# Kernel optimization log

Hardware: AMD Instinct MI355X
Metric: run time of the kernel (lower is better)

The kernel has to match this reference:

```python
import jax, jax.numpy as jnp
import numpy as np

N_NODES = 100000
E_HALF = 2000000  # edges come in two mirrored halves (two classes per node pair)
IN_DIM, HID = 5, 16


def setup_inputs() -> dict:
    key = jax.random.key(0)
    ks = jax.random.split(key, 8)
    x = jax.random.normal(ks[0], (N_NODES, IN_DIM), dtype=jnp.float32)
    e_half = jax.random.randint(ks[1], (2, E_HALF), 0, N_NODES)
    edges = jnp.concatenate([e_half, e_half], axis=1)  # [2, 2*E_HALF]
    edge_attr = jax.random.uniform(ks[2], (2 * E_HALF, 2), dtype=jnp.float32)
    detector_labels = jax.random.bernoulli(ks[3], 0.5, (N_NODES,))
    s = 1.0 / np.sqrt(IN_DIM)
    W_rel = jax.random.uniform(ks[4], (HID, IN_DIM), minval=-s, maxval=s, dtype=jnp.float32)
    b_rel = jax.random.uniform(ks[5], (HID,), minval=-s, maxval=s, dtype=jnp.float32)
    W_root = jax.random.uniform(ks[6], (HID, IN_DIM), minval=-s, maxval=s, dtype=jnp.float32)
    s2 = 1.0 / np.sqrt(2 * HID + 1)
    k7, k8 = jax.random.split(ks[7])
    W_lin = jax.random.uniform(k7, (1, 2 * HID + 1), minval=-s2, maxval=s2, dtype=jnp.float32)
    b_lin = jax.random.uniform(k8, (1,), minval=-s2, maxval=s2, dtype=jnp.float32)
    return {
        "x": x, "edges": edges, "edge_attr": edge_attr,
        "detector_labels": detector_labels,
        "W_rel": W_rel, "b_rel": b_rel, "W_root": W_root,
        "W_lin": W_lin, "b_lin": b_lin,
    }


def reference(x, edges, edge_attr, detector_labels, W_rel, b_rel, W_root, W_lin, b_lin):
    N = x.shape[0]
    src, dst = edges[0], edges[1]
    # GraphConv(aggr='add'): out_i = W_root x_i + W_rel * sum_{(j->i)} w_e * x_j + b_rel
    w = edge_attr[:, 1]
    msg = x[src] * w[:, None]                                  # [E, 5]
    agg = jax.ops.segment_sum(msg, dst, num_segments=N)        # [N, 5]
    h = jnp.tanh(agg @ W_rel.T + b_rel + x @ W_root.T)         # [N, 16]
    # SplitSyndromes: keep edges whose both endpoints are detector nodes
    valid = detector_labels[src] & detector_labels[dst]
    vidx = jnp.nonzero(valid)[0]                               # data-dependent (eager)
    e = edges[:, vidx]
    ea = edge_attr[vidx]
    # gather-concat-linear edge scoring
    feat = jnp.concatenate([h[e[0]], ea[:, :1], h[e[1]]], axis=-1)  # [nv, 33]
    score = feat @ W_lin.T + b_lin                             # [nv, 1]
    nv = score.shape[0]
    half = nv // 2
    score2 = score.reshape(-1, half)                           # [2, half]
    classes2 = ea[:, 1].reshape(-1, half)
    mi = jnp.argmin(score2, axis=0)
    cols = jnp.arange(half)
    return e[:, :half], score2[mi, cols], classes2[mi, cols]
```

## Files before the change

kernel.cpp:

```cpp
#include <hip/hip_runtime.h>

#define HID 16
#define IN_DIM 5
#define PAD 8
#define EPT 4
#define EPB (256 * EPT)

#define FXS 64.0f
#define FXI 0.015625f

__device__ __forceinline__ float decode_field(unsigned long long& T) {
    int r = (int)(T & 0xFFFull);
    int s = (r >= 2048) ? r - 4096 : r;
    T = (T - (unsigned long long)(long long)s) >> 12;
    return (float)s * FXI;
}

__device__ __forceinline__ void scan256(const int* __restrict__ counts,
                                        int* __restrict__ offs, int nbv) {
    __shared__ int wS[4];
    int tid = threadIdx.x;
    int base = tid * 8;
    int vals[8];
    int tsum = 0;
#pragma unroll
    for (int k = 0; k < 8; k++) {
        int idx = base + k;
        vals[k] = (idx < nbv) ? counts[idx] : 0;
        tsum += vals[k];
    }
    int lane = tid & 63, wid = tid >> 6;
    int scan = tsum;
#pragma unroll
    for (int off = 1; off < 64; off <<= 1) {
        int u = __shfl_up(scan, off, 64);
        if (lane >= off) scan += u;
    }
    if (lane == 63) wS[wid] = scan;
    __syncthreads();
    int waveBase = 0;
#pragma unroll
    for (int k = 0; k < 4; k++) if (k < wid) waveBase += wS[k];
    int excl = waveBase + scan - tsum;
#pragma unroll
    for (int k = 0; k < 8; k++) {
        int idx = base + k;
        if (idx < nbv) offs[idx] = excl;
        excl += vals[k];
    }
}

__device__ __forceinline__ void gridbar(int* bar, int G) {
    __syncthreads();
    if (threadIdx.x == 0) {
        __threadfence();
        __hip_atomic_fetch_add(bar, 1, __ATOMIC_ACQ_REL, __HIP_MEMORY_SCOPE_AGENT);
        while (__hip_atomic_load(bar, __ATOMIC_ACQUIRE, __HIP_MEMORY_SCOPE_AGENT) < G)
            __builtin_amdgcn_s_sleep(32);
        __threadfence();
    }
    __syncthreads();
}

__global__ __launch_bounds__(256) void fused(
        const float* __restrict__ x, const int* __restrict__ src,
        const int* __restrict__ dst, const float2* __restrict__ ea2,
        const int* __restrict__ lab,
        const float* __restrict__ Wrel, const float* __restrict__ brel,
        const float* __restrict__ Wroot, const float* __restrict__ Wlin,
        const float* __restrict__ blin,
        unsigned long long* __restrict__ agg, float2* __restrict__ uvp,
        int* __restrict__ counts, int* __restrict__ offs,
        float4* __restrict__ st4, float* __restrict__ out,
        int* __restrict__ bars,
        int N, int EH, int K, int nbv) {
    const int tid = threadIdx.x;
    const int G = gridDim.x;
    const int GT = G * 256;
    const int gt = blockIdx.x * 256 + tid;
    const int lane = tid & 63, wid = tid >> 6;

    __shared__ float sWrel[HID * IN_DIM];
    __shared__ float sWroot[HID * IN_DIM];
    __shared__ float sBrel[HID];
    __shared__ float sWl[2 * HID + 1];
    if (tid < HID * IN_DIM) sWrel[tid] = Wrel[tid];
    else if (tid < 2 * HID * IN_DIM) sWroot[tid - HID * IN_DIM] = Wroot[tid - HID * IN_DIM];
    else if (tid < 2 * HID * IN_DIM + HID) sBrel[tid - 2 * HID * IN_DIM] = brel[tid - 2 * HID * IN_DIM];
    else if (tid < 2 * HID * IN_DIM + HID + 2 * HID + 1)
        sWl[tid - 2 * HID * IN_DIM - HID] = Wlin[tid - 2 * HID * IN_DIM - HID];

    float w16 = Wlin[HID];
    __shared__ int wc[4];
    for (int vb = blockIdx.x; vb < nbv; vb += G) {
        const int i0 = vb * EPB + tid * EPT;
        int s[EPT], d[EPT];
        float2 eaA[EPT], eaB[EPT];
        bool act[EPT];
        if (i0 + EPT <= EH) {
            int4 s4 = *(const int4*)(src + i0);
            int4 d4 = *(const int4*)(dst + i0);
            s[0] = s4.x; s[1] = s4.y; s[2] = s4.z; s[3] = s4.w;
            d[0] = d4.x; d[1] = d4.y; d[2] = d4.z; d[3] = d4.w;
            float4 a0 = *(const float4*)(ea2 + i0);
            float4 a1 = *(const float4*)(ea2 + i0 + 2);
            float4 b0 = *(const float4*)(ea2 + (size_t)i0 + EH);
            float4 b1 = *(const float4*)(ea2 + (size_t)i0 + EH + 2);
            eaA[0] = make_float2(a0.x, a0.y); eaA[1] = make_float2(a0.z, a0.w);
            eaA[2] = make_float2(a1.x, a1.y); eaA[3] = make_float2(a1.z, a1.w);
            eaB[0] = make_float2(b0.x, b0.y); eaB[1] = make_float2(b0.z, b0.w);
            eaB[2] = make_float2(b1.x, b1.y); eaB[3] = make_float2(b1.z, b1.w);
#pragma unroll
            for (int k = 0; k < EPT; k++) act[k] = true;
        } else {
#pragma unroll
            for (int k = 0; k < EPT; k++) {
                int i = i0 + k;
                act[k] = (i < EH);
                s[k] = act[k] ? src[i] : 0;
                d[k] = act[k] ? dst[i] : 0;
                eaA[k] = act[k] ? ea2[i] : make_float2(0.f, 0.f);
                eaB[k] = act[k] ? ea2[(size_t)i + EH] : make_float2(0.f, 0.f);
            }
        }
        bool ld[EPT], vl[EPT];
#pragma unroll
        for (int k = 0; k < EPT; k++) {
            bool ls = lab[s[k]] != 0;
            bool lv = lab[d[k]] != 0;
            ld[k] = act[k] && lv;
            vl[k] = ld[k] && ls;
        }
#pragma unroll
        for (int k = 0; k < EPT; k++) {
            if (ld[k]) {
                const float* xs = x + (size_t)s[k] * IN_DIM;
                float4 xa = *(const float4*)xs;
                float  x4 = xs[4];
                float w = (eaA[k].y + eaB[k].y) * FXS;
                unsigned long long a = 0;
                int q0 = __float2int_rn(xa.x * w);
                int q1 = __float2int_rn(xa.y * w);
                int q2 = __float2int_rn(xa.z * w);
                int q3 = __float2int_rn(xa.w * w);
                int q4 = __float2int_rn(x4 * w);
                a += (unsigned long long)(long long)q0;
                a += (unsigned long long)(long long)q1 << 12;
                a += (unsigned long long)(long long)q2 << 24;
                a += (unsigned long long)(long long)q3 << 36;
                a += (unsigned long long)(long long)q4 << 48;
                atomicAdd(&agg[(size_t)d[k] * PAD], a);
            }
        }
        float scpart[EPT], cls[EPT];
#pragma unroll
        for (int k = 0; k < EPT; k++) {
            float p0 = w16 * eaA[k].x;
            float p1 = w16 * eaB[k].x;
            if (p1 < p0) { scpart[k] = p1; cls[k] = eaB[k].y; }
            else         { scpart[k] = p0; cls[k] = eaA[k].y; }
        }
        unsigned m4 = 0;
#pragma unroll
        for (int k = 0; k < EPT; k++) m4 |= (vl[k] ? (1u << k) : 0u);
        int cnt = __popc(m4);
        int scan = cnt;
#pragma unroll
        for (int off = 1; off < 64; off <<= 1) {
            int u = __shfl_up(scan, off, 64);
            if (lane >= off) scan += u;
        }
        __syncthreads();
        if (lane == 63) wc[wid] = scan;
        __syncthreads();
        if (tid == 0) counts[vb] = wc[0] + wc[1] + wc[2] + wc[3];
        int wexcl = 0;
#pragma unroll
        for (int k = 0; k < 4; k++) if (k < wid) wexcl += wc[k];
        int idx = vb * EPB + wexcl + (scan - cnt);
#pragma unroll
        for (int k = 0; k < EPT; k++) {
            if (vl[k]) {
                float4 r;
                r.x = __int_as_float(s[k]);
                r.y = __int_as_float(d[k]);
                r.z = scpart[k];
                r.w = cls[k];
                st4[idx++] = r;
            }
        }
    }
    gridbar(&bars[0], G);

    if (blockIdx.x == 0) scan256(counts, offs, nbv);
    {
        int iters = (N + GT - 1) / GT;
        for (int it = 0; it < iters; ++it) {
            int n = gt + it * GT;
            if (n < N && lab[n]) {
                unsigned long long T = agg[(size_t)n * PAD];
                float a[IN_DIM], xv[IN_DIM];
#pragma unroll
                for (int dd = 0; dd < IN_DIM; dd++) a[dd] = decode_field(T);
#pragma unroll
                for (int dd = 0; dd < IN_DIM; dd++) xv[dd] = x[(size_t)n * IN_DIM + dd];
                float u = 0.f, vv = 0.f;
#pragma unroll
                for (int kk = 0; kk < HID; kk++) {
                    float acc = sBrel[kk];
#pragma unroll
                    for (int dd = 0; dd < IN_DIM; dd++)
                        acc += a[dd] * sWrel[kk * IN_DIM + dd] + xv[dd] * sWroot[kk * IN_DIM + dd];
                    float hk = tanhf(acc);
                    u += sWl[kk] * hk;
                    vv += sWl[HID + 1 + kk] * hk;
                }
                uvp[n] = make_float2(u, vv);
            }
        }
    }
    gridbar(&bars[16], G);

    float bl = blin[0];
    const float* uvf = (const float*)uvp;
    for (int vb = blockIdx.x; vb < nbv; vb += G) {
        int cnt = counts[vb];
        int base = offs[vb];
        for (int t = tid; t < cnt; t += 256) {
            float4 r = st4[(size_t)vb * EPB + t];
            int s = __float_as_int(r.x);
            int d = __float_as_int(r.y);
            float sc = bl + uvf[2 * (size_t)s] + uvf[2 * (size_t)d + 1] + r.z;
            int ro = base + t;
            out[ro] = (float)s;
            out[(size_t)K + ro] = (float)d;
            out[2 * (size_t)K + ro] = sc;
            out[3 * (size_t)K + ro] = r.w;
        }
    }
}

__global__ void pack_labels(const int* __restrict__ lab, const float* __restrict__ x,
                            unsigned long long* __restrict__ bits, float* __restrict__ xp,
                            int N) {
    int n = blockIdx.x * 256 + threadIdx.x;
    bool p = (n < N) && (lab[n] != 0);
    unsigned long long m = __ballot(p);
    if (((threadIdx.x & 63) == 0) && n < N) bits[n >> 6] = m;
    if (n < N) {
        float4 a;
        a.x = x[(size_t)n * IN_DIM + 0];
        a.y = x[(size_t)n * IN_DIM + 1];
        a.z = x[(size_t)n * IN_DIM + 2];
        a.w = x[(size_t)n * IN_DIM + 3];
        *(float4*)(xp + (size_t)n * 8) = a;
        float4 b;
        b.x = x[(size_t)n * IN_DIM + 4];
        b.y = 0.f; b.z = 0.f; b.w = 0.f;
        *(float4*)(xp + (size_t)n * 8 + 4) = b;
    }
}

__global__ __launch_bounds__(256, 4) void scatter_count(
        const int* __restrict__ src, const int* __restrict__ dst,
        const unsigned long long* __restrict__ bits,
        const float2* __restrict__ ea2,
        const float* __restrict__ xp,
        const float* __restrict__ Wlin,
        unsigned long long* __restrict__ agg,
        int* __restrict__ counts,
        float4* __restrict__ st4,
        int EH) {
    const int tid = threadIdx.x;
    const int i0 = (blockIdx.x * 256 + tid) * EPT;
    int s[EPT], d[EPT];
    float2 eaA[EPT], eaB[EPT];
    bool act[EPT];
    if (i0 + EPT <= EH) {
        int4 s4 = *(const int4*)(src + i0);
        int4 d4 = *(const int4*)(dst + i0);
        s[0] = s4.x; s[1] = s4.y; s[2] = s4.z; s[3] = s4.w;
        d[0] = d4.x; d[1] = d4.y; d[2] = d4.z; d[3] = d4.w;
        float4 a0 = *(const float4*)(ea2 + i0);
        float4 a1 = *(const float4*)(ea2 + i0 + 2);
        float4 b0 = *(const float4*)(ea2 + (size_t)i0 + EH);
        float4 b1 = *(const float4*)(ea2 + (size_t)i0 + EH + 2);
        eaA[0] = make_float2(a0.x, a0.y); eaA[1] = make_float2(a0.z, a0.w);
        eaA[2] = make_float2(a1.x, a1.y); eaA[3] = make_float2(a1.z, a1.w);
        eaB[0] = make_float2(b0.x, b0.y); eaB[1] = make_float2(b0.z, b0.w);
        eaB[2] = make_float2(b1.x, b1.y); eaB[3] = make_float2(b1.z, b1.w);
#pragma unroll
        for (int k = 0; k < EPT; k++) act[k] = true;
    } else {
#pragma unroll
        for (int k = 0; k < EPT; k++) {
            int i = i0 + k;
            act[k] = (i < EH);
            s[k] = act[k] ? src[i] : 0;
            d[k] = act[k] ? dst[i] : 0;
            eaA[k] = act[k] ? ea2[i] : make_float2(0.f, 0.f);
            eaB[k] = act[k] ? ea2[(size_t)i + EH] : make_float2(0.f, 0.f);
        }
    }
    bool ld[EPT], vl[EPT];
#pragma unroll
    for (int k = 0; k < EPT; k++) {
        bool ls = (bits[s[k] >> 6] >> (s[k] & 63)) & 1;
        bool lv = (bits[d[k] >> 6] >> (d[k] & 63)) & 1;
        ld[k] = act[k] && lv;
        vl[k] = ld[k] && ls;
    }
#pragma unroll
    for (int k = 0; k < EPT; k++) {
        if (ld[k]) {
            const float* xs = xp + (size_t)s[k] * 8;
            float4 xa = *(const float4*)xs;
            float  x4 = xs[4];
            float w = (eaA[k].y + eaB[k].y) * FXS;
            unsigned long long a = 0;
            int q0 = __float2int_rn(xa.x * w);
            int q1 = __float2int_rn(xa.y * w);
            int q2 = __float2int_rn(xa.z * w);
            int q3 = __float2int_rn(xa.w * w);
            int q4 = __float2int_rn(x4 * w);
            a += (unsigned long long)(long long)q0;
            a += (unsigned long long)(long long)q1 << 12;
            a += (unsigned long long)(long long)q2 << 24;
            a += (unsigned long long)(long long)q3 << 36;
            a += (unsigned long long)(long long)q4 << 48;
            atomicAdd(&agg[(size_t)d[k] * PAD], a);
        }
    }
    float w16 = Wlin[HID];
    float scpart[EPT], cls[EPT];
#pragma unroll
    for (int k = 0; k < EPT; k++) {
        float p0 = w16 * eaA[k].x;
        float p1 = w16 * eaB[k].x;
        if (p1 < p0) { scpart[k] = p1; cls[k] = eaB[k].y; }
        else         { scpart[k] = p0; cls[k] = eaA[k].y; }
    }
    unsigned m4 = 0;
#pragma unroll
    for (int k = 0; k < EPT; k++) m4 |= (vl[k] ? (1u << k) : 0u);
    int cnt = __popc(m4);
    int lane = tid & 63, wid = tid >> 6;
    int scan = cnt;
#pragma unroll
    for (int off = 1; off < 64; off <<= 1) {
        int u = __shfl_up(scan, off, 64);
        if (lane >= off) scan += u;
    }
    __shared__ int wc[4];
    if (lane == 63) wc[wid] = scan;
    __syncthreads();
    if (tid == 0) counts[blockIdx.x] = wc[0] + wc[1] + wc[2] + wc[3];
    int wexcl = 0;
#pragma unroll
    for (int k = 0; k < 4; k++) if (k < wid) wexcl += wc[k];
    int idx = blockIdx.x * EPB + wexcl + (scan - cnt);
#pragma unroll
    for (int k = 0; k < EPT; k++) {
        if (vl[k]) {
            float4 r;
            r.x = __int_as_float(s[k]);
            r.y = __int_as_float(d[k]);
            r.z = scpart[k];
            r.w = cls[k];
            st4[idx++] = r;
        }
    }
}

__global__ void compute_uv(const float* __restrict__ xp,
                           const unsigned long long* __restrict__ agg,
                           const int* __restrict__ lab,
                           const float* __restrict__ Wrel, const float* __restrict__ brel,
                           const float* __restrict__ Wroot, const float* __restrict__ Wlin,
                           float2* __restrict__ uv, int N) {
    __shared__ float sWrel[HID * IN_DIM];
    __shared__ float sWroot[HID * IN_DIM];
    __shared__ float sBrel[HID];
    __shared__ float sWl[2 * HID + 1];
    int t = threadIdx.x;
    if (t < HID * IN_DIM) sWrel[t] = Wrel[t];
    else if (t < 2 * HID * IN_DIM) sWroot[t - HID * IN_DIM] = Wroot[t - HID * IN_DIM];
    else if (t < 2 * HID * IN_DIM + HID) sBrel[t - 2 * HID * IN_DIM] = brel[t - 2 * HID * IN_DIM];
    else if (t < 2 * HID * IN_DIM + HID + 2 * HID + 1)
        sWl[t - 2 * HID * IN_DIM - HID] = Wlin[t - 2 * HID * IN_DIM - HID];
    __syncthreads();
    int n = blockIdx.x * 256 + threadIdx.x;
    if (n >= N) return;
    if (!lab[n]) return;
    unsigned long long T = agg[(size_t)n * PAD];
    float a[IN_DIM], xv[IN_DIM];
#pragma unroll
    for (int d = 0; d < IN_DIM; d++) a[d] = decode_field(T);
    float4 x0 = *(const float4*)(xp + (size_t)n * 8);
    xv[0] = x0.x; xv[1] = x0.y; xv[2] = x0.z; xv[3] = x0.w;
    xv[4] = xp[(size_t)n * 8 + 4];
    float u = 0.f, vv = 0.f;
#pragma unroll
    for (int k = 0; k < HID; k++) {
        float acc = sBrel[k];
#pragma unroll
        for (int d = 0; d < IN_DIM; d++)
            acc += a[d] * sWrel[k * IN_DIM + d] + xv[d] * sWroot[k * IN_DIM + d];
        float hk = tanhf(acc);
        u += sWl[k] * hk;
        vv += sWl[HID + 1 + k] * hk;
    }
    uv[n] = make_float2(u, vv);
}

__global__ void scan_counts(const int* __restrict__ counts, int* __restrict__ offs, int nb) {
    __shared__ int waveSums[16];
    int tid = threadIdx.x;
    int base = tid * 8;
    int vals[8];
    int tsum = 0;
#pragma unroll
    for (int k = 0; k < 8; k++) {
        int idx = base + k;
        vals[k] = (idx < nb) ? counts[idx] : 0;
        tsum += vals[k];
    }
    int lane = tid & 63, wid = tid >> 6;
    int scan = tsum;
#pragma unroll
    for (int off = 1; off < 64; off <<= 1) {
        int u = __shfl_up(scan, off, 64);
        if (lane >= off) scan += u;
    }
    if (lane == 63) waveSums[wid] = scan;
    __syncthreads();
    if (wid == 0 && lane < 16) {
        int s = waveSums[lane];
#pragma unroll
        for (int off = 1; off < 16; off <<= 1) {
            int u = __shfl_up(s, off, 64);
            if (lane >= off) s += u;
        }
        waveSums[lane] = s;
    }
    __syncthreads();
    int waveBase = (wid > 0) ? waveSums[wid - 1] : 0;
    int excl = waveBase + scan - tsum;
#pragma unroll
    for (int k = 0; k < 8; k++) {
        int idx = base + k;
        if (idx < nb) offs[idx] = excl;
        excl += vals[k];
    }
}

__global__ void emit_out(const float4* __restrict__ st4,
                         const float* __restrict__ uvf, const float* __restrict__ blin,
                         const int* __restrict__ counts, const int* __restrict__ offs,
                         float* __restrict__ out, int K) {
    int b = blockIdx.x;
    int cnt = counts[b];
    int base = offs[b];
    float bl = blin[0];
    for (int t = threadIdx.x; t < cnt; t += 256) {
        float4 r = st4[(size_t)b * EPB + t];
        int s = __float_as_int(r.x);
        int d = __float_as_int(r.y);
        float sc = bl + uvf[2 * (size_t)s] + uvf[2 * (size_t)d + 1] + r.z;
        int ro = base + t;
        out[ro] = (float)s;
        out[(size_t)K + ro] = (float)d;
        out[2 * (size_t)K + ro] = sc;
        out[3 * (size_t)K + ro] = r.w;
    }
}

extern "C" void kernel_launch(void* const* d_in, const int* in_sizes, int n_in,
                              void* d_out, int out_size, void* d_ws, size_t ws_size,
                              hipStream_t stream) {
    const float* x     = (const float*)d_in[0];
    const int*   edges = (const int*)d_in[1];
    const float* ea    = (const float*)d_in[2];
    const int*   lab   = (const int*)d_in[3];
    const float* Wrel  = (const float*)d_in[4];
    const float* brel  = (const float*)d_in[5];
    const float* Wroot = (const float*)d_in[6];
    const float* Wlin  = (const float*)d_in[7];
    const float* blin  = (const float*)d_in[8];

    int N  = in_sizes[0] / IN_DIM;
    const int E  = in_sizes[1] / 2;
    int EH = E / 2;
    int K  = out_size / 4;

    const int* src = edges;
    const int* dst = edges + E;
    const float2* ea2 = (const float2*)ea;
    int nbv = (EH + EPB - 1) / EPB;
    const int nslots = nbv * EPB;

    char* ws = (char*)d_ws;
    size_t off = 0;
    unsigned long long* agg = (unsigned long long*)(ws + off); off += (size_t)N * PAD * 8;
    int* bars = (int*)(ws + off); off += 256;
    float2* uv = (float2*)(ws + off); off += (size_t)N * 8;
    unsigned long long* bits = (unsigned long long*)(ws + off);
    off += (size_t)(((N + 63) / 64) * 8 + 255) / 256 * 256;
    float* xp = (float*)(ws + off); off += (size_t)N * 8 * 4;
    int* counts = (int*)(ws + off); off += (size_t)(nbv * 4 + 255) / 256 * 256;
    int* offs   = (int*)(ws + off); off += (size_t)(nbv * 4 + 255) / 256 * 256;
    float4* st4 = (float4*)(ws + off); off += (size_t)nslots * 16;

    float* out = (float*)d_out;

    static int G = 0;
    if (G == 0) {
        int bpc = 0;
        hipError_t e = hipOccupancyMaxActiveBlocksPerMultiprocessor(&bpc, fused, 256, 0);
        int dev = 0;
        hipGetDevice(&dev);
        hipDeviceProp_t prop;
        hipGetDeviceProperties(&prop, dev);
        int cu = prop.multiProcessorCount;
        if (e != hipSuccess || bpc < 1 || cu < 1 || nbv > 2048) {
            G = -1;
        } else {
            long g = ((long)bpc * cu) / 2;
            if (g < cu) g = cu;
            if (g > 2048) g = 2048;
            G = (int)g;
        }
    }

    if (G > 0) {
        hipMemsetAsync(agg, 0, (size_t)N * PAD * 8 + 256, stream);
        fused<<<G, 256, 0, stream>>>(x, src, dst, ea2, lab, Wrel, brel, Wroot, Wlin, blin,
                                     agg, uv, counts, offs, st4, out, bars, N, EH, K, nbv);
    } else {
        hipMemsetAsync(agg, 0, (size_t)N * PAD * 8, stream);
        pack_labels<<<(N + 255) / 256, 256, 0, stream>>>(lab, x, bits, xp, N);
        scatter_count<<<nbv, 256, 0, stream>>>(src, dst, bits, ea2, xp, Wlin, agg, counts,
                                               st4, EH);
        compute_uv<<<(N + 255) / 256, 256, 0, stream>>>(xp, agg, lab, Wrel, brel, Wroot, Wlin, uv, N);
        scan_counts<<<1, 1024, 0, stream>>>(counts, offs, nbv);
        emit_out<<<nbv, 256, 0, stream>>>(st4, (const float*)uv, blin, counts, offs, out, K);
    }
}
```

Baseline: 178.6 us.

## Fold agg zeroing and label bit-packing into fused kernel with extra grid barrier

The agg buffer is now zeroed and detector labels are packed into a 64-bit bitmask inside the persistent kernel, behind a new grid barrier, replacing the large host-issued memset with a small one covering only the barrier counters. Label lookups in the edge loop and in the node pass use the compact bitmask, which improves cache hit rates for random gathers. The grid size is raised to the full occupancy-derived value (capped at the number of edge blocks), launch bounds request 6 blocks per unit, and the barrier spin sleep is shortened. The cost is an extra grid-wide barrier and possible register pressure from the occupancy hint.

Measured after the change: 640.9 us. +258.7%, slower.

```diff
diff --git a/kernel.cpp b/kernel.cpp
--- a/kernel.cpp
+++ b/kernel.cpp
@@ -56,13 +56,13 @@
         __threadfence();
         __hip_atomic_fetch_add(bar, 1, __ATOMIC_ACQ_REL, __HIP_MEMORY_SCOPE_AGENT);
         while (__hip_atomic_load(bar, __ATOMIC_ACQUIRE, __HIP_MEMORY_SCOPE_AGENT) < G)
-            __builtin_amdgcn_s_sleep(32);
+            __builtin_amdgcn_s_sleep(8);
         __threadfence();
     }
     __syncthreads();
 }
 
-__global__ __launch_bounds__(256) void fused(
+__global__ __launch_bounds__(256, 6) void fused(
         const float* __restrict__ x, const int* __restrict__ src,
         const int* __restrict__ dst, const float2* __restrict__ ea2,
         const int* __restrict__ lab,
@@ -70,6 +70,7 @@
         const float* __restrict__ Wroot, const float* __restrict__ Wlin,
         const float* __restrict__ blin,
         unsigned long long* __restrict__ agg, float2* __restrict__ uvp,
+        unsigned long long* __restrict__ bits,
         int* __restrict__ counts, int* __restrict__ offs,
         float4* __restrict__ st4, float* __restrict__ out,
         int* __restrict__ bars,
@@ -89,6 +90,21 @@
     else if (tid < 2 * HID * IN_DIM + HID) sBrel[tid - 2 * HID * IN_DIM] = brel[tid - 2 * HID * IN_DIM];
     else if (tid < 2 * HID * IN_DIM + HID + 2 * HID + 1)
         sWl[tid - 2 * HID * IN_DIM - HID] = Wlin[tid - 2 * HID * IN_DIM - HID];
+
+    {
+        size_t tot = (size_t)N * (PAD / 2);
+        ulonglong2 z; z.x = 0ull; z.y = 0ull;
+        for (size_t i = (size_t)gt; i < tot; i += GT) ((ulonglong2*)agg)[i] = z;
+        int iters = (N + GT - 1) / GT;
+        for (int it = 0; it < iters; ++it) {
+            int n = gt + it * GT;
+            bool in = n < N;
+            bool p = in && (lab[n] != 0);
+            unsigned long long m = __ballot(p);
+            if (lane == 0 && in) bits[n >> 6] = m;
+        }
+    }
+    gridbar(&bars[0], G);
 
     float w16 = Wlin[HID];
     __shared__ int wc[4];
@@ -126,8 +142,8 @@
         bool ld[EPT], vl[EPT];
 #pragma unroll
         for (int k = 0; k < EPT; k++) {
-            bool ls = lab[s[k]] != 0;
-            bool lv = lab[d[k]] != 0;
+            bool ls = (bits[s[k] >> 6] >> (s[k] & 63)) & 1;
+            bool lv = (bits[d[k] >> 6] >> (d[k] & 63)) & 1;
             ld[k] = act[k] && lv;
             vl[k] = ld[k] && ls;
         }
@@ -190,14 +206,14 @@
             }
         }
     }
-    gridbar(&bars[0], G);
+    gridbar(&bars[16], G);
 
     if (blockIdx.x == 0) scan256(counts, offs, nbv);
     {
         int iters = (N + GT - 1) / GT;
         for (int it = 0; it < iters; ++it) {
             int n = gt + it * GT;
-            if (n < N && lab[n]) {
+            if (n < N && (((bits[n >> 6] >> (n & 63)) & 1) != 0)) {
                 unsigned long long T = agg[(size_t)n * PAD];
                 float a[IN_DIM], xv[IN_DIM];
 #pragma unroll
@@ -219,7 +235,7 @@
             }
         }
     }
-    gridbar(&bars[16], G);
+    gridbar(&bars[32], G);
 
     float bl = blin[0];
     const float* uvf = (const float*)uvp;
@@ -525,17 +541,18 @@
         if (e != hipSuccess || bpc < 1 || cu < 1 || nbv > 2048) {
             G = -1;
         } else {
-            long g = ((long)bpc * cu) / 2;
-            if (g < cu) g = cu;
+            long g = (long)bpc * cu;
             if (g > 2048) g = 2048;
+            if (g > nbv) g = nbv;
             G = (int)g;
         }
     }
 
     if (G > 0) {
-        hipMemsetAsync(agg, 0, (size_t)N * PAD * 8 + 256, stream);
+        hipMemsetAsync(bars, 0, 256, stream);
         fused<<<G, 256, 0, stream>>>(x, src, dst, ea2, lab, Wrel, brel, Wroot, Wlin, blin,
-                                     agg, uv, counts, offs, st4, out, bars, N, EH, K, nbv);
+                                     agg, uv, bits, counts, offs, st4, out, bars,
+                                     N, EH, K, nbv);
     } else {
         hipMemsetAsync(agg, 0, (size_t)N * PAD * 8, stream);
         pack_labels<<<(N + 255) / 256, 256, 0, stream>>>(lab, x, bits, xp, N);
```
